# Kernel optimization log

Measured on AMD Instinct MI355X. Metric: run time of the kernel, lower is better.

The kernel has to match this reference:

```python
import jax, jax.numpy as jnp
import numpy as np

# dims
B, C, H, W = 8, 256, 64, 128
P = 4                      # patch size (p1 == p2)
E = C // 2                 # embed dim = ngf//2 = Mamba d_model
HP, WP = H // P, W // P
N = HP * WP                # 512 tokens
DM = E                     # Mamba d_model
DI = 2 * DM                # d_inner (expand=2)
DS = 16                    # d_state
DC = 4                     # d_conv
DR = DM // 16              # dt_rank
NG = 128                   # new_ngf
S = 2                      # pixel-shuffle stride


def setup_inputs() -> dict:
    key = jax.random.key(0)
    ks = jax.random.split(key, 16)
    g = lambda i, shape, s=0.02: jax.random.normal(ks[i], shape, jnp.float32) * s
    return {
        'x': jax.random.normal(ks[0], (B, C, H, W), jnp.float32),
        # patch embed (conv k=stride=P)
        'patch_w': g(1, (E, C, P, P)),
        'patch_b': jnp.zeros((E,), jnp.float32),
        # Mamba params
        'in_proj_w': g(2, (2 * DI, DM)),
        'conv1d_w': g(3, (DI, DC), 0.1),
        'conv1d_b': jnp.zeros((DI,), jnp.float32),
        'x_proj_w': g(4, (DR + 2 * DS, DI)),
        'dt_proj_w': g(5, (DI, DR), 0.1),
        'dt_proj_b': jnp.full((DI,), -3.0, jnp.float32),
        'A_log': jnp.log(jnp.broadcast_to(jnp.arange(1, DS + 1, dtype=jnp.float32), (DI, DS))),
        'D_param': jnp.ones((DI,), jnp.float32),
        'out_proj_w': g(6, (DM, DI)),
        # unpatchify linear N -> N*P*P
        'lin_w': g(7, (N * P * P, N)),
        'lin_b': jnp.zeros((N * P * P,), jnp.float32),
        # nerv conv (3x3, out = new_ngf*S*S)
        'conv_w': g(8, (NG * S * S, E, 3, 3), 0.05),
        'conv_b': jnp.zeros((NG * S * S,), jnp.float32),
        # residual FFN (1x1)
        'ffn_w1': g(9, (NG, NG)),
        'ffn_b1': jnp.zeros((NG,), jnp.float32),
        'ffn_w2': g(10, (NG, NG)),
        'ffn_b2': jnp.zeros((NG,), jnp.float32),
    }


def reference(x, patch_w, patch_b, in_proj_w, conv1d_w, conv1d_b, x_proj_w,
              dt_proj_w, dt_proj_b, A_log, D_param, out_proj_w, lin_w, lin_b,
              conv_w, conv_b, ffn_w1, ffn_b1, ffn_w2, ffn_b2):
    silu = jax.nn.silu
    # ---- patch embed: (B,C,H,W) -> (B,N,E)
    t = jax.lax.conv_general_dilated(x, patch_w, (P, P), 'VALID',
                                     dimension_numbers=('NCHW', 'OIHW', 'NCHW'))
    t = t + patch_b[None, :, None, None]
    t = t.reshape(B, E, N).transpose(0, 2, 1)  # (B,N,E)

    # ---- Mamba selective scan
    xz = jnp.einsum('bld,ed->ble', t, in_proj_w)      # (B,N,2*DI)
    xin, z = jnp.split(xz, 2, axis=-1)
    # depthwise causal conv1d over sequence
    xp = jnp.pad(xin, ((0, 0), (DC - 1, 0), (0, 0)))
    xc = sum(xp[:, k:k + N, :] * conv1d_w[:, k] for k in range(DC)) + conv1d_b
    xc = silu(xc)                                     # (B,N,DI)
    dbl = jnp.einsum('bld,ed->ble', xc, x_proj_w)
    dt, Bs, Cs = dbl[..., :DR], dbl[..., DR:DR + DS], dbl[..., DR + DS:]
    dt = jax.nn.softplus(jnp.einsum('blr,dr->bld', dt, dt_proj_w) + dt_proj_b)
    A = -jnp.exp(A_log)                               # (DI,DS)
    dA = jnp.exp(dt[..., None] * A)                   # (B,N,DI,DS)
    dBx = dt[..., None] * Bs[:, :, None, :] * xc[..., None]

    def step(h, inputs):
        dA_t, dBx_t, C_t = inputs
        h = dA_t * h + dBx_t                          # (B,DI,DS)
        y = jnp.einsum('bdn,bn->bd', h, C_t)
        return h, y

    h0 = jnp.zeros((B, DI, DS), xc.dtype)
    _, ys = jax.lax.scan(step, h0, (dA.transpose(1, 0, 2, 3),
                                    dBx.transpose(1, 0, 2, 3),
                                    Cs.transpose(1, 0, 2)))
    y = ys.transpose(1, 0, 2) + D_param * xc
    y = y * silu(z)
    out = jnp.einsum('bld,ed->ble', y, out_proj_w)    # (B,N,DM)

    # ---- unpatchify: (B,N,E) -> (B,E,H,W)
    u = out.transpose(0, 2, 1)                        # (B,E,N)
    u = jnp.einsum('ben,mn->bem', u, lin_w) + lin_b   # (B,E,N*P*P)
    u = u.reshape(B, E, HP, WP, P, P).transpose(0, 1, 2, 4, 3, 5)
    u = u.reshape(B, E, H, W)

    # ---- nerv block: 3x3 conv -> pixel shuffle -> gelu
    c = jax.lax.conv_general_dilated(u, conv_w, (1, 1), ((1, 1), (1, 1)),
                                     dimension_numbers=('NCHW', 'OIHW', 'NCHW'))
    c = c + conv_b[None, :, None, None]               # (B,NG*S*S,H,W)
    c = c.reshape(B, NG, S, S, H, W).transpose(0, 1, 4, 2, 5, 3)
    c = c.reshape(B, NG, H * S, W * S)
    c = jax.nn.gelu(c)

    # ---- residual FFN (1x1 convs over channels)
    f = jax.nn.gelu(jnp.einsum('bchw,ec->behw', c, ffn_w1) + ffn_b1[None, :, None, None])
    f = jnp.einsum('behw,ce->bchw', f, ffn_w2) + ffn_b2[None, :, None, None]
    return c + f
```

## Files before the change

### kernel.cpp

```cpp
#include <hip/hip_runtime.h>
#include <hip/hip_bf16.h>

#define HW2 32768

typedef __attribute__((ext_vector_type(8))) short short8v;
typedef __attribute__((ext_vector_type(4))) float f32x4;

__device__ __forceinline__ float siluf(float x){ return x / (1.f + __expf(-x)); }
__device__ __forceinline__ float geluf(float v){
  float t = 0.7978845608028654f * fmaf(0.044715f*v*v, v, v);
  t = fminf(fmaxf(t, -15.f), 15.f);
  float e = __expf(2.f*t);
  return 0.5f*v*(1.f + (e-1.f)/(e+1.f));
}
__device__ __forceinline__ ushort bf16rne(float f){
  unsigned u = __float_as_uint(f);
  unsigned r = (u + 0x7fffu + ((u >> 16) & 1u)) >> 16;
  return (ushort)r;
}
__device__ __forceinline__ float bf2f(ushort u){ return __uint_as_float(((unsigned)u) << 16); }
__device__ __forceinline__ void split2(float v, ushort& h, ushort& lo){
  h = bf16rne(v);
  lo = bf16rne(v - bf2f(h));
}

__global__ __launch_bounds__(256) void k_zero4(uint4* __restrict__ p, int n){
  int i = blockIdx.x*256 + threadIdx.x;
  if (i < n) p[i] = make_uint4(0,0,0,0);
}

__global__ __launch_bounds__(256) void k_wprep(const float* __restrict__ cw, ushort* __restrict__ wbf){
  int idx = blockIdx.x*256 + threadIdx.x;
  int j    = idx & 7;
  int lane = (idx >> 3) & 63;
  int f    = (idx >> 9) & 3;
  int tap  = (idx >> 11) % 9;
  int rest = idx / 18432;
  int ec = rest & 3, ocg = rest >> 2;
  int o = ocg*64 + f*16 + (lane & 15);
  int e = ec*32 + (lane >> 4)*8 + j;
  float v = cw[((size_t)o*128 + e)*9 + tap];
  wbf[idx] = bf16rne(v);
}

__global__ __launch_bounds__(256) void k_wffn(const float* __restrict__ w1, const float* __restrict__ w2,
                                              ushort* __restrict__ wpad){
  int idx = blockIdx.x*256 + threadIdx.x;
  int which = idx / 17408;
  int rem = idx - which*17408;
  int e = rem / 136, k = rem - e*136;
  const float* s = which ? w2 : w1;
  wpad[idx] = (k < 128) ? bf16rne(s[e*128 + k]) : (ushort)0;
}

__global__ __launch_bounds__(256) void k_wlin(const float* __restrict__ lw, ushort* __restrict__ lwbf){
  int i = blockIdx.x*256 + threadIdx.x;
  float4 v = reinterpret_cast<const float4*>(lw)[i];
  uint2 u;
  u.x = (uint)bf16rne(v.x) | ((uint)bf16rne(v.y) << 16);
  u.y = (uint)bf16rne(v.z) | ((uint)bf16rne(v.w) << 16);
  reinterpret_cast<uint2*>(lwbf)[i] = u;
}

__global__ __launch_bounds__(256) void k_ytr(const float* __restrict__ yo, ushort* __restrict__ ybfT){
  __shared__ float tile[32][132];
  int b = blockIdx.x, n0 = blockIdx.y*32;
  int tid = threadIdx.x;
  for (int it = 0; it < 16; ++it) {
    int idx = it*256 + tid;
    int row = idx >> 7, e = idx & 127;
    tile[row][e] = yo[((size_t)(b*512 + n0 + row))*128 + e];
  }
  __syncthreads();
  int e = tid >> 1, half = tid & 1;
  uint* dst = reinterpret_cast<uint*>(ybfT + ((size_t)b*128 + e)*512 + n0 + half*16);
  #pragma unroll
  for (int j = 0; j < 8; ++j) {
    int n = half*16 + j*2;
    dst[j] = (uint)bf16rne(tile[n][e]) | ((uint)bf16rne(tile[n+1][e]) << 16);
  }
}

__global__ __launch_bounds__(256) void k_patchm(const float* __restrict__ x, const float* __restrict__ pw,
                                                float* __restrict__ part){
  __shared__ ushort Ah[4096], Al[4096], Wh[4096], Wl[4096];
  int m0 = blockIdx.x * 128;
  int ks = blockIdx.y;
  int tid = threadIdx.x;
  int l = tid & 63, wv = tid >> 6;
  int wm = wv >> 1, we = wv & 1;
  int lj = l & 15, lg = l >> 4;
  f32x4 acc[4][4];
  #pragma unroll
  for (int a = 0; a < 4; ++a)
    #pragma unroll
    for (int b = 0; b < 4; ++b)
      acc[a][b] = (f32x4){0.f,0.f,0.f,0.f};
  int kbase = ks * 512;

  for (int it = 0; it < 16; ++it) {
    int k0 = kbase + it*32;
    __syncthreads();
    #pragma unroll
    for (int q = 0; q < 4; ++q) {
      int flat = q*256 + tid;
      int row = flat & 127, kk4 = flat >> 7;
      int m = m0 + row;
      int bb = m >> 9, ll = m & 511;
      int hp = ll >> 5, wp = ll & 31;
      int k = k0 + kk4*4;
      int c = k >> 4, i2 = (k >> 2) & 3;
      float4 v = *reinterpret_cast<const float4*>(x + (((bb*256 + c)*64 + hp*4 + i2)*128 + wp*4));
      ushort h0,h1,h2,h3,q0,q1,q2,q3;
      split2(v.x,h0,q0); split2(v.y,h1,q1); split2(v.z,h2,q2); split2(v.w,h3,q3);
      uint2 uh, ul;
      uh.x = (uint)h0 | ((uint)h1 << 16); uh.y = (uint)h2 | ((uint)h3 << 16);
      ul.x = (uint)q0 | ((uint)q1 << 16); ul.y = (uint)q2 | ((uint)q3 << 16);
      int lane = ((kk4 >> 1) << 4) | (row & 15);
      int dst = ((row >> 4)*64 + lane)*8 + (kk4 & 1)*4;
      *reinterpret_cast<uint2*>(Ah + dst) = uh;
      *reinterpret_cast<uint2*>(Al + dst) = ul;
    }
    #pragma unroll
    for (int q = 0; q < 4; ++q) {
      int flat = q*256 + tid;
      int e = flat >> 3, kk4 = flat & 7;
      float4 v = *reinterpret_cast<const float4*>(pw + (size_t)e*4096 + k0 + kk4*4);
      ushort h0,h1,h2,h3,q0,q1,q2,q3;
      split2(v.x,h0,q0); split2(v.y,h1,q1); split2(v.z,h2,q2); split2(v.w,h3,q3);
      uint2 uh, ul;
      uh.x = (uint)h0 | ((uint)h1 << 16); uh.y = (uint)h2 | ((uint)h3 << 16);
      ul.x = (uint)q0 | ((uint)q1 << 16); ul.y = (uint)q2 | ((uint)q3 << 16);
      int lane = ((kk4 >> 1) << 4) | (e & 15);
      int dst = ((e >> 4)*64 + lane)*8 + (kk4 & 1)*4;
      *reinterpret_cast<uint2*>(Wh + dst) = uh;
      *reinterpret_cast<uint2*>(Wl + dst) = ul;
    }
    __syncthreads();

    short8v ah[4], al_[4], wh[4], wl_[4];
    #pragma unroll
    for (int f = 0; f < 4; ++f) {
      ah[f]  = *reinterpret_cast<const short8v*>(Ah + ((wm*4 + f)*64 + l)*8);
      al_[f] = *reinterpret_cast<const short8v*>(Al + ((wm*4 + f)*64 + l)*8);
      wh[f]  = *reinterpret_cast<const short8v*>(Wh + ((we*4 + f)*64 + l)*8);
      wl_[f] = *reinterpret_cast<const short8v*>(Wl + ((we*4 + f)*64 + l)*8);
    }
    #pragma unroll
    for (int fo = 0; fo < 4; ++fo)
      #pragma unroll
      for (int fj = 0; fj < 4; ++fj) {
        acc[fo][fj] = __builtin_amdgcn_mfma_f32_16x16x32_bf16(ah[fo],  wh[fj],  acc[fo][fj], 0, 0, 0);
        acc[fo][fj] = __builtin_amdgcn_mfma_f32_16x16x32_bf16(ah[fo],  wl_[fj], acc[fo][fj], 0, 0, 0);
        acc[fo][fj] = __builtin_amdgcn_mfma_f32_16x16x32_bf16(al_[fo], wh[fj],  acc[fo][fj], 0, 0, 0);
      }
  }
  float* pb = part + (size_t)ks*524288;
  #pragma unroll
  for (int fo = 0; fo < 4; ++fo) {
    int m = m0 + wm*64 + fo*16 + lg*4;
    #pragma unroll
    for (int fj = 0; fj < 4; ++fj) {
      int e = we*64 + fj*16 + lj;
      f32x4 a = acc[fo][fj];
      pb[(size_t)(m+0)*128 + e] = a.x;
      pb[(size_t)(m+1)*128 + e] = a.y;
      pb[(size_t)(m+2)*128 + e] = a.z;
      pb[(size_t)(m+3)*128 + e] = a.w;
    }
  }
}

__global__ __launch_bounds__(256) void k_tred(const float* __restrict__ part, const float* __restrict__ pb,
                                              float* __restrict__ t){
  int i = blockIdx.x*256 + threadIdx.x;
  const float4* p4 = reinterpret_cast<const float4*>(part);
  float4 s = reinterpret_cast<const float4*>(pb)[i & 31];
  #pragma unroll
  for (int ks = 0; ks < 8; ++ks) {
    float4 v = p4[(size_t)ks*131072 + i];
    s.x += v.x; s.y += v.y; s.z += v.z; s.w += v.w;
  }
  reinterpret_cast<float4*>(t)[i] = s;
}

__global__ __launch_bounds__(256) void k_gemm(const float* __restrict__ A, const float* __restrict__ W,
                                              float* __restrict__ C, int M, int N, int K){
  __shared__ __align__(16) float As[16][68];
  __shared__ __align__(16) float Bs[16][68];
  int m0 = blockIdx.x * 64, n0 = blockIdx.y * 64;
  int tid = threadIdx.x;
  int tm = tid >> 4, tn = tid & 15;
  int lm = tid >> 2, kq = tid & 3;
  float acc[4][4] = {};
  const float* Abase = A + (size_t)(m0 + lm)*K + kq*4;
  const float* Wbase = W + (size_t)(n0 + lm)*K + kq*4;
  for (int k0 = 0; k0 < K; k0 += 16) {
    float4 av = *reinterpret_cast<const float4*>(Abase + k0);
    float4 bv = *reinterpret_cast<const float4*>(Wbase + k0);
    As[kq*4+0][lm]=av.x; As[kq*4+1][lm]=av.y; As[kq*4+2][lm]=av.z; As[kq*4+3][lm]=av.w;
    Bs[kq*4+0][lm]=bv.x; Bs[kq*4+1][lm]=bv.y; Bs[kq*4+2][lm]=bv.z; Bs[kq*4+3][lm]=bv.w;
    __syncthreads();
    #pragma unroll
    for (int kk = 0; kk < 16; ++kk) {
      float4 a = *reinterpret_cast<const float4*>(&As[kk][tm*4]);
      float4 b = *reinterpret_cast<const float4*>(&Bs[kk][tn*4]);
      float ar[4] = {a.x,a.y,a.z,a.w};
      float br[4] = {b.x,b.y,b.z,b.w};
      #pragma unroll
      for (int i = 0; i < 4; ++i)
        #pragma unroll
        for (int j = 0; j < 4; ++j)
          acc[i][j] = fmaf(ar[i], br[j], acc[i][j]);
    }
    __syncthreads();
  }
  #pragma unroll
  for (int i = 0; i < 4; ++i) {
    float4 ov = make_float4(acc[i][0], acc[i][1], acc[i][2], acc[i][3]);
    *reinterpret_cast<float4*>(C + (size_t)(m0 + tm*4 + i)*N + n0 + tn*4) = ov;
  }
}

__global__ __launch_bounds__(256) void k_conv1d(const float* __restrict__ xz, const float* __restrict__ w,
                                                const float* __restrict__ bias, float* __restrict__ xc){
  int idx = blockIdx.x*256 + threadIdx.x;
  int d = idx & 255;
  int l = (idx >> 8) & 511;
  int bb = idx >> 17;
  const float* base = xz + (size_t)bb*512*512 + d;
  float s = bias[d];
  #pragma unroll
  for (int k = 0; k < 4; ++k) {
    int ls = l - 3 + k;
    if (ls >= 0) s = fmaf(base[(size_t)ls*512], w[d*4+k], s);
  }
  xc[idx] = s / (1.f + __expf(-s));
}

__global__ __launch_bounds__(256) void k_xproj(const float* __restrict__ xc, const float* __restrict__ xpw,
                                               const float* __restrict__ dtw, const float* __restrict__ dtb,
                                               float* __restrict__ dbl, float* __restrict__ dt){
  __shared__ __align__(16) float sxc[256];
  __shared__ float sdbl[40];
  int bl = blockIdx.x;
  int tid = threadIdx.x;
  sxc[tid] = xc[(size_t)bl*256 + tid];
  __syncthreads();
  if (tid < 40) {
    const float4* wr = reinterpret_cast<const float4*>(xpw + tid*256);
    const float4* xr = reinterpret_cast<const float4*>(sxc);
    float s = 0.f;
    #pragma unroll 8
    for (int i = 0; i < 64; ++i) {
      float4 w = wr[i], xv = xr[i];
      s += w.x*xv.x + w.y*xv.y + w.z*xv.z + w.w*xv.w;
    }
    sdbl[tid] = s;
    dbl[(size_t)bl*40 + tid] = s;
  }
  __syncthreads();
  float s = dtb[tid];
  const float* wr = dtw + tid*8;
  #pragma unroll
  for (int r = 0; r < 8; ++r) s = fmaf(sdbl[r], wr[r], s);
  float sp = (s > 20.f) ? s : log1pf(__expf(s));
  dt[(size_t)bl*256 + tid] = sp;
}

__global__ __launch_bounds__(256) void k_scanA(const float* __restrict__ dt, const float* __restrict__ dbl,
                                               const float* __restrict__ xc, const float* __restrict__ A_log,
                                               float* __restrict__ aprod, float* __restrict__ hend){
  __shared__ float sdt[32][16], sxc[32][16], sB[32][16];
  int tid = threadIdx.x;
  int bg = blockIdx.x;
  int ch = blockIdx.y;
  int bb = bg >> 4, dgrp = bg & 15;
  int l0 = ch*32;
  #pragma unroll
  for (int it = 0; it < 2; ++it) {
    int idx = it*256 + tid;
    int t = idx >> 4, dd = idx & 15;
    int base = bb*512 + l0 + t;
    sdt[t][dd] = dt[(size_t)base*256 + dgrp*16 + dd];
    sxc[t][dd] = xc[(size_t)base*256 + dgrp*16 + dd];
    sB [t][dd] = dbl[(size_t)base*40 + 8 + dd];
  }
  __syncthreads();
  int n = tid & 15, dloc = tid >> 4;
  float Ac = -__expf(A_log[(dgrp*16 + dloc)*16 + n]);
  float a = 1.f, h = 0.f;
  #pragma unroll
  for (int t = 0; t < 32; ++t) {
    float dtv = sdt[t][dloc], xcv = sxc[t][dloc], Bv = sB[t][n];
    float dA = __expf(dtv*Ac);
    h = fmaf(dA, h, dtv*Bv*xcv);
    a *= dA;
  }
  aprod[(size_t)(bg*16 + ch)*256 + tid] = a;
  hend [(size_t)(bg*16 + ch)*256 + tid] = h;
}

__global__ __launch_bounds__(256) void k_scanB(const float* __restrict__ aprod, const float* __restrict__ hend,
                                               float* __restrict__ hstart){
  int tid = threadIdx.x;
  int bg = blockIdx.x;
  float hs = 0.f;
  #pragma unroll
  for (int ch = 0; ch < 16; ++ch) {
    size_t idx = (size_t)(bg*16 + ch)*256 + tid;
    hstart[idx] = hs;
    hs = fmaf(aprod[idx], hs, hend[idx]);
  }
}

__global__ __launch_bounds__(256) void k_scanC(const float* __restrict__ dt, const float* __restrict__ dbl,
                                               const float* __restrict__ xc, const float* __restrict__ xz,
                                               const float* __restrict__ A_log, const float* __restrict__ Dp,
                                               const float* __restrict__ hstart, float* __restrict__ y){
  __shared__ float sdt[32][16], sxc[32][16], sB[32][16], sC[32][16], sz[32][16];
  int tid = threadIdx.x;
  int bg = blockIdx.x;
  int ch = blockIdx.y;
  int bb = bg >> 4, dgrp = bg & 15;
  int l0 = ch*32;
  #pragma unroll
  for (int it = 0; it < 2; ++it) {
    int idx = it*256 + tid;
    int t = idx >> 4, dd = idx & 15;
    int base = bb*512 + l0 + t;
    sdt[t][dd] = dt[(size_t)base*256 + dgrp*16 + dd];
    sxc[t][dd] = xc[(size_t)base*256 + dgrp*16 + dd];
    sB [t][dd] = dbl[(size_t)base*40 + 8  + dd];
    sC [t][dd] = dbl[(size_t)base*40 + 24 + dd];
    sz [t][dd] = xz[(size_t)base*512 + 256 + dgrp*16 + dd];
  }
  __syncthreads();
  int n = tid & 15, dloc = tid >> 4;
  int d = dgrp*16 + dloc;
  float Ac = -__expf(A_log[d*16 + n]);
  float Dv = Dp[d];
  float h = hstart[(size_t)(bg*16 + ch)*256 + tid];
  #pragma unroll 4
  for (int t = 0; t < 32; ++t) {
    float dtv = sdt[t][dloc], xcv = sxc[t][dloc];
    float Bv = sB[t][n], Cv = sC[t][n];
    float dA = __expf(dtv*Ac);
    h = fmaf(dA, h, dtv*Bv*xcv);
    float yp = h*Cv;
    yp += __shfl_xor(yp, 1, 16);
    yp += __shfl_xor(yp, 2, 16);
    yp += __shfl_xor(yp, 4, 16);
    yp += __shfl_xor(yp, 8, 16);
    if (n == 0) {
      float zv = sz[t][dloc];
      y[(size_t)(bb*512 + l0 + t)*256 + d] = (yp + Dv*xcv) * (zv / (1.f + __expf(-zv)));
    }
  }
}

__global__ __launch_bounds__(512) void k_linm(const ushort* __restrict__ ybfT, const ushort* __restrict__ lwbf,
                                              const float* __restrict__ lb, ushort* __restrict__ ubf){
  __shared__ ushort As[128*88];
  __shared__ ushort Bs[128*88];
  int m0 = blockIdx.x * 128;
  int b  = blockIdx.y;
  int tid = threadIdx.x;
  int l = tid & 63, wv = tid >> 6;
  int wm = wv & 3, we = wv >> 2;
  int lj = l & 15, lg = l >> 4;
  f32x4 acc[4][2];
  #pragma unroll
  for (int fo = 0; fo < 4; ++fo)
    #pragma unroll
    for (int fj = 0; fj < 2; ++fj)
      acc[fo][fj] = (f32x4){0.f,0.f,0.f,0.f};

  for (int k0 = 0; k0 < 512; k0 += 64) {
    __syncthreads();
    #pragma unroll
    for (int it = 0; it < 2; ++it) {
      int flat = it*512 + tid;
      int e = flat >> 3, kc8 = flat & 7;
      *reinterpret_cast<uint4*>(&As[e*88 + kc8*8]) =
        *reinterpret_cast<const uint4*>(ybfT + ((size_t)b*128 + e)*512 + k0 + kc8*8);
      *reinterpret_cast<uint4*>(&Bs[e*88 + kc8*8]) =
        *reinterpret_cast<const uint4*>(lwbf + (size_t)(m0 + e)*512 + k0 + kc8*8);
    }
    __syncthreads();
    #pragma unroll
    for (int kc = 0; kc < 2; ++kc) {
      short8v af[4], bq[2];
      #pragma unroll
      for (int fo = 0; fo < 4; ++fo)
        af[fo] = *reinterpret_cast<const short8v*>(&As[(we*64 + fo*16 + lj)*88 + kc*32 + lg*8]);
      #pragma unroll
      for (int fj = 0; fj < 2; ++fj)
        bq[fj] = *reinterpret_cast<const short8v*>(&Bs[(wm*32 + fj*16 + lj)*88 + kc*32 + lg*8]);
      #pragma unroll
      for (int fo = 0; fo < 4; ++fo)
        #pragma unroll
        for (int fj = 0; fj < 2; ++fj)
          acc[fo][fj] = __builtin_amdgcn_mfma_f32_16x16x32_bf16(af[fo], bq[fj], acc[fo][fj], 0, 0, 0);
    }
  }
  #pragma unroll
  for (int fj = 0; fj < 2; ++fj) {
    int m = m0 + wm*32 + fj*16 + lj;
    float bias = lb[m];
    int hh = ((m >> 9) << 2) + ((m >> 2) & 3);
    int ww = (((m >> 4) & 31) << 2) + (m & 3);
    #pragma unroll
    for (int fo = 0; fo < 4; ++fo) {
      int eg = we*2 + (fo >> 1);
      int e5 = ((fo & 1) << 4) + (lg << 2);
      f32x4 a = acc[fo][fj];
      uint2 u;
      u.x = (uint)bf16rne(a.x + bias) | ((uint)bf16rne(a.y + bias) << 16);
      u.y = (uint)bf16rne(a.z + bias) | ((uint)bf16rne(a.w + bias) << 16);
      *reinterpret_cast<uint2*>(ubf + ((((size_t)b*4 + eg)*66 + hh + 1)*130 + ww + 1)*32 + e5) = u;
    }
  }
}

__global__ __launch_bounds__(256, 3) void k_conv3m(const ushort* __restrict__ ubf, const ushort* __restrict__ wbf,
                                                   const float* __restrict__ cb, float* __restrict__ out){
  __shared__ ushort wlds[18432];
  int h2 = blockIdx.x;
  int bz = blockIdx.y;
  int bb = bz >> 3, ocg = bz & 7;
  int tid = threadIdx.x;
  int l   = tid & 63;
  int wv  = tid >> 6;
  int hr  = wv >> 1;
  int wseg = (wv & 1) * 64;
  int lj = l & 15, lg = l >> 4;

  f32x4 acc[4][4];
  #pragma unroll
  for (int i = 0; i < 4; ++i)
    #pragma unroll
    for (int j = 0; j < 4; ++j)
      acc[i][j] = (f32x4){0.f, 0.f, 0.f, 0.f};

  for (int ec = 0; ec < 4; ++ec) {
    __syncthreads();
    const uint4* sA = reinterpret_cast<const uint4*>(wbf) + (size_t)(ocg*4 + ec)*2304;
    uint4* dA = reinterpret_cast<uint4*>(wlds);
    #pragma unroll
    for (int q = 0; q < 9; ++q) dA[q*256 + tid] = sA[q*256 + tid];
    __syncthreads();

    const ushort* ub_ec = ubf + (((size_t)(bb*4 + ec)*66 + 2*h2 + hr)*130 + wseg + lj)*32 + lg*8;
    #pragma unroll
    for (int ki = 0; ki < 3; ++ki) {
      const ushort* bbase = ub_ec + (size_t)ki*4160;
      #pragma unroll
      for (int kj = 0; kj < 3; ++kj) {
        const ushort* wtap = wlds + (ki*3 + kj)*2048 + l*8;
        short8v af[4], bfr[4];
        #pragma unroll
        for (int f = 0; f < 4; ++f)
          af[f] = *reinterpret_cast<const short8v*>(wtap + f*512);
        #pragma unroll
        for (int f = 0; f < 4; ++f)
          bfr[f] = *reinterpret_cast<const short8v*>(bbase + (f*16 + kj)*32);
        #pragma unroll
        for (int fo = 0; fo < 4; ++fo)
          #pragma unroll
          for (int fj = 0; fj < 4; ++fj)
            acc[fo][fj] = __builtin_amdgcn_mfma_f32_16x16x32_bf16(af[fo], bfr[fj], acc[fo][fj], 0, 0, 0);
      }
    }
  }

  int row = h2*2 + hr;
  #pragma unroll
  for (int fo = 0; fo < 4; ++fo) {
    int obase = ocg*64 + fo*16 + lg*4;
    int g = obase >> 2;
    float b0 = cb[obase], b1 = cb[obase+1], b2 = cb[obase+2], b3 = cb[obase+3];
    size_t rbase0 = (((size_t)bb*128 + g)*128 + 2*row)*256;
    size_t rbase1 = rbase0 + 256;
    #pragma unroll
    for (int fj = 0; fj < 4; ++fj) {
      int w = wseg + fj*16 + lj;
      f32x4 a = acc[fo][fj];
      float2 v0 = make_float2(geluf(a.x + b0), geluf(a.y + b1));
      float2 v1 = make_float2(geluf(a.z + b2), geluf(a.w + b3));
      *reinterpret_cast<float2*>(out + rbase0 + 2*w) = v0;
      *reinterpret_cast<float2*>(out + rbase1 + 2*w) = v1;
    }
  }
}

__global__ __launch_bounds__(512) void k_ffnm(const ushort* __restrict__ wpad, const float* __restrict__ b1,
                                              const float* __restrict__ b2, float* __restrict__ io){
  extern __shared__ ushort sm[];
  ushort* cT = sm;
  ushort* wl = sm + 128*136;
  int pix0 = blockIdx.x * 128;
  int bb = pix0 >> 15;
  int hw0 = pix0 & 32767;
  int tid = threadIdx.x;
  int l = tid & 63, wv = tid >> 6;
  int wc = wv >> 2, wp = wv & 3;
  int lj = l & 15, lg = l >> 4;
  int r = tid & 1, hpair = tid >> 1;
  const float* cbase = io + (size_t)bb*128*HW2 + hw0;

  for (int it = 0; it < 16; ++it) {
    int flat = it*256 + hpair;
    int pp = flat & 63;
    int cpair = flat >> 6;
    int ch = cpair*2 + r;
    float2 v = *reinterpret_cast<const float2*>(cbase + (size_t)ch*HW2 + pp*2);
    float oa = __shfl_xor(v.x, 1);
    float ob = __shfl_xor(v.y, 1);
    ushort lo = r ? bf16rne(ob) : bf16rne(v.x);
    ushort hi = r ? bf16rne(v.y) : bf16rne(oa);
    *reinterpret_cast<uint*>(&cT[(pp*2 + r)*136 + cpair*2]) = (uint)lo | ((uint)hi << 16);
  }
  {
    const uint4* src = reinterpret_cast<const uint4*>(wpad);
    uint4* dst = reinterpret_cast<uint4*>(wl);
    for (int i = tid; i < 2176; i += 512) dst[i] = src[i];
  }
  __syncthreads();

  f32x4 acc[4][2];
  #pragma unroll
  for (int fo = 0; fo < 4; ++fo)
    #pragma unroll
    for (int fj = 0; fj < 2; ++fj)
      acc[fo][fj] = (f32x4){0.f,0.f,0.f,0.f};

  #pragma unroll
  for (int kc = 0; kc < 4; ++kc) {
    short8v af[4], bq[2];
    #pragma unroll
    for (int fo = 0; fo < 4; ++fo)
      af[fo] = *reinterpret_cast<const short8v*>(&wl[(wc*64 + fo*16 + lj)*136 + kc*32 + lg*8]);
    #pragma unroll
    for (int fj = 0; fj < 2; ++fj)
      bq[fj] = *reinterpret_cast<const short8v*>(&cT[(wp*32 + fj*16 + lj)*136 + kc*32 + lg*8]);
    #pragma unroll
    for (int fo = 0; fo < 4; ++fo)
      #pragma unroll
      for (int fj = 0; fj < 2; ++fj)
        acc[fo][fj] = __builtin_amdgcn_mfma_f32_16x16x32_bf16(af[fo], bq[fj], acc[fo][fj], 0, 0, 0);
  }
  __syncthreads();

  const ushort* w2g = wpad + 17408;
  short8v a2[4], a2n[4];
  #pragma unroll
  for (int fo = 0; fo < 4; ++fo)
    a2[fo] = *reinterpret_cast<const short8v*>(w2g + (size_t)(wc*64 + fo*16 + lj)*136 + lg*8);

  #pragma unroll
  for (int fo = 0; fo < 4; ++fo) {
    int ch0 = wc*64 + fo*16 + lg*4;
    float c0 = b1[ch0], c1 = b1[ch0+1], c2 = b1[ch0+2], c3 = b1[ch0+3];
    #pragma unroll
    for (int fj = 0; fj < 2; ++fj) {
      int px = wp*32 + fj*16 + lj;
      f32x4 a = acc[fo][fj];
      uint2 u;
      u.x = (uint)bf16rne(geluf(a.x + c0)) | ((uint)bf16rne(geluf(a.y + c1)) << 16);
      u.y = (uint)bf16rne(geluf(a.z + c2)) | ((uint)bf16rne(geluf(a.w + c3)) << 16);
      *reinterpret_cast<uint2*>(&wl[px*136 + ch0]) = u;
    }
  }
  __syncthreads();

  #pragma unroll
  for (int fo = 0; fo < 4; ++fo)
    #pragma unroll
    for (int fj = 0; fj < 2; ++fj)
      acc[fo][fj] = (f32x4){0.f,0.f,0.f,0.f};

  #pragma unroll
  for (int kc = 0; kc < 4; ++kc) {
    if (kc < 3) {
      #pragma unroll
      for (int fo = 0; fo < 4; ++fo)
        a2n[fo] = *reinterpret_cast<const short8v*>(w2g + (size_t)(wc*64 + fo*16 + lj)*136 + (kc+1)*32 + lg*8);
    }
    short8v bq[2];
    #pragma unroll
    for (int fj = 0; fj < 2; ++fj)
      bq[fj] = *reinterpret_cast<const short8v*>(&wl[(wp*32 + fj*16 + lj)*136 + kc*32 + lg*8]);
    #pragma unroll
    for (int fo = 0; fo < 4; ++fo)
      #pragma unroll
      for (int fj = 0; fj < 2; ++fj)
        acc[fo][fj] = __builtin_amdgcn_mfma_f32_16x16x32_bf16(a2[fo], bq[fj], acc[fo][fj], 0, 0, 0);
    #pragma unroll
    for (int fo = 0; fo < 4; ++fo) a2[fo] = a2n[fo];
  }

  #pragma unroll
  for (int fo = 0; fo < 4; ++fo) {
    int ch0 = wc*64 + fo*16 + lg*4;
    float d0 = b2[ch0], d1 = b2[ch0+1], d2 = b2[ch0+2], d3 = b2[ch0+3];
    #pragma unroll
    for (int fj = 0; fj < 2; ++fj) {
      int px = wp*32 + fj*16 + lj;
      f32x4 a = acc[fo][fj];
      uint2 cu = *reinterpret_cast<const uint2*>(&cT[px*136 + ch0]);
      float cv0 = __uint_as_float((cu.x & 0xffffu) << 16);
      float cv1 = __uint_as_float(cu.x & 0xffff0000u);
      float cv2 = __uint_as_float((cu.y & 0xffffu) << 16);
      float cv3 = __uint_as_float(cu.y & 0xffff0000u);
      float* p0 = io + (size_t)bb*128*HW2 + (size_t)ch0*HW2 + hw0 + px;
      p0[0]             = cv0 + a.x + d0;
      p0[HW2]           = cv1 + a.y + d1;
      p0[2*HW2]         = cv2 + a.z + d2;
      p0[3*(size_t)HW2] = cv3 + a.w + d3;
    }
  }
}

extern "C" void kernel_launch(void* const* d_in, const int* in_sizes, int n_in,
                              void* d_out, int out_size, void* d_ws, size_t ws_size,
                              hipStream_t stream) {
  const float* x          = (const float*)d_in[0];
  const float* patch_w    = (const float*)d_in[1];
  const float* patch_b    = (const float*)d_in[2];
  const float* in_proj_w  = (const float*)d_in[3];
  const float* conv1d_w   = (const float*)d_in[4];
  const float* conv1d_b   = (const float*)d_in[5];
  const float* x_proj_w   = (const float*)d_in[6];
  const float* dt_proj_w  = (const float*)d_in[7];
  const float* dt_proj_b  = (const float*)d_in[8];
  const float* A_log      = (const float*)d_in[9];
  const float* D_param    = (const float*)d_in[10];
  const float* out_proj_w = (const float*)d_in[11];
  const float* lin_w      = (const float*)d_in[12];
  const float* lin_b      = (const float*)d_in[13];
  const float* conv_w     = (const float*)d_in[14];
  const float* conv_b     = (const float*)d_in[15];
  const float* ffn_w1     = (const float*)d_in[16];
  const float* ffn_b1     = (const float*)d_in[17];
  const float* ffn_w2     = (const float*)d_in[18];
  const float* ffn_b2     = (const float*)d_in[19];
  float* out = (float*)d_out;
  float* ws  = (float*)d_ws;

  float* t    = ws;
  float* xz   = t    + 524288;
  float* xc   = xz   + 2097152;
  float* dbl  = xc   + 1048576;
  float* dt   = dbl  + 163840;
  float* y    = dt   + 1048576;
  float* yo   = y    + 1048576;
  float* apr  = yo   + 524288;
  float* hend = apr  + 524288;
  float* hst  = hend + 524288;
  ushort* ubf  = (ushort*)(hst + 524288);
  ushort* wbf  = ubf + 10982400;
  ushort* wpad = wbf + 589824;
  ushort* lwbf = wpad + 34816;
  ushort* ybfT = lwbf + 4194304;
  float* part = xz;

  k_zero4 <<<dim3(5363), dim3(256), 0, stream>>>((uint4*)ubf, 1372800);
  k_wprep <<<dim3(2304), dim3(256), 0, stream>>>(conv_w, wbf);
  k_wffn  <<<dim3(136), dim3(256), 0, stream>>>(ffn_w1, ffn_w2, wpad);
  k_wlin  <<<dim3(4096), dim3(256), 0, stream>>>(lin_w, lwbf);
  k_patchm<<<dim3(32, 8), dim3(256), 0, stream>>>(x, patch_w, part);
  k_tred  <<<dim3(512), dim3(256), 0, stream>>>(part, patch_b, t);
  k_gemm  <<<dim3(64, 8), dim3(256), 0, stream>>>(t, in_proj_w, xz, 4096, 512, 128);
  k_conv1d<<<dim3(4096), dim3(256), 0, stream>>>(xz, conv1d_w, conv1d_b, xc);
  k_xproj <<<dim3(4096), dim3(256), 0, stream>>>(xc, x_proj_w, dt_proj_w, dt_proj_b, dbl, dt);
  k_scanA <<<dim3(128, 16), dim3(256), 0, stream>>>(dt, dbl, xc, A_log, apr, hend);
  k_scanB <<<dim3(128), dim3(256), 0, stream>>>(apr, hend, hst);
  k_scanC <<<dim3(128, 16), dim3(256), 0, stream>>>(dt, dbl, xc, xz, A_log, D_param, hst, y);
  k_gemm  <<<dim3(64, 2), dim3(256), 0, stream>>>(y, out_proj_w, yo, 4096, 128, 256);
  k_ytr   <<<dim3(8, 16), dim3(256), 0, stream>>>(yo, ybfT);
  k_linm  <<<dim3(64, 8), dim3(512), 0, stream>>>(ybfT, lwbf, lin_b, ubf);
  k_conv3m<<<dim3(32, 64), dim3(256), 0, stream>>>(ubf, wbf, conv_b, out);
  k_ffnm  <<<dim3(2048), dim3(512), (size_t)(2*128*136)*sizeof(ushort), stream>>>(wpad, ffn_b1, ffn_b2, out);
}
```

Measured before the change: 344.9 us.

## Write conv output as bf16 intermediate, split conv+FFN into batch halves

The 3x3 conv now writes its gelu output as bf16 into a workspace buffer instead of fp32 into the final output, and the FFN reads that bf16 buffer and writes the final fp32 result. This halves conv write traffic and FFN read traffic and may keep the intermediate resident in cache. Conv and FFN run in two batch halves of four so the intermediate is smaller. The full zeroing of the padded buffer is replaced by a kernel that zeroes only the halo border, and conv launch bounds rise to four blocks per SM. The result is unchanged in value, because the FFN already rounded its input to bf16.

```diff
diff --git a/kernel.cpp b/kernel.cpp
--- a/kernel.cpp
+++ b/kernel.cpp
@@ -24,9 +24,23 @@
   lo = bf16rne(v - bf2f(h));
 }
 
-__global__ __launch_bounds__(256) void k_zero4(uint4* __restrict__ p, int n){
-  int i = blockIdx.x*256 + threadIdx.x;
-  if (i < n) p[i] = make_uint4(0,0,0,0);
+__global__ __launch_bounds__(256) void k_zb(uint4* __restrict__ ubf4){
+  int bid = blockIdx.x;
+  int tid = threadIdx.x;
+  uint4 z = make_uint4(0,0,0,0);
+  size_t base4 = (size_t)bid * 34320;
+  for (int i = tid; i < 1552; i += 256) {
+    size_t off;
+    if (i < 520)       off = i;
+    else if (i < 1040) off = 33800 + (i - 520);
+    else {
+      int j = i - 1040;
+      int row = 1 + (j >> 3);
+      int colsel = (j >> 2) & 1, q = j & 3;
+      off = (size_t)row*520 + colsel*516 + q;
+    }
+    ubf4[base4 + off] = z;
+  }
 }
 
 __global__ __launch_bounds__(256) void k_wprep(const float* __restrict__ cw, ushort* __restrict__ wbf){
@@ -423,12 +437,14 @@
   }
 }
 
-__global__ __launch_bounds__(256, 3) void k_conv3m(const ushort* __restrict__ ubf, const ushort* __restrict__ wbf,
-                                                   const float* __restrict__ cb, float* __restrict__ out){
+__global__ __launch_bounds__(256, 4) void k_conv3m(const ushort* __restrict__ ubf, const ushort* __restrict__ wbf,
+                                                   const float* __restrict__ cb, ushort* __restrict__ cbf,
+                                                   int bbase){
   __shared__ ushort wlds[18432];
   int h2 = blockIdx.x;
   int bz = blockIdx.y;
-  int bb = bz >> 3, ocg = bz & 7;
+  int bbl = bz >> 3, ocg = bz & 7;
+  int bb = bbase + bbl;
   int tid = threadIdx.x;
   int l   = tid & 63;
   int wv  = tid >> 6;
@@ -454,7 +470,7 @@
     const ushort* ub_ec = ubf + (((size_t)(bb*4 + ec)*66 + 2*h2 + hr)*130 + wseg + lj)*32 + lg*8;
     #pragma unroll
     for (int ki = 0; ki < 3; ++ki) {
-      const ushort* bbase = ub_ec + (size_t)ki*4160;
+      const ushort* bbase_p = ub_ec + (size_t)ki*4160;
       #pragma unroll
       for (int kj = 0; kj < 3; ++kj) {
         const ushort* wtap = wlds + (ki*3 + kj)*2048 + l*8;
@@ -464,7 +480,7 @@
           af[f] = *reinterpret_cast<const short8v*>(wtap + f*512);
         #pragma unroll
         for (int f = 0; f < 4; ++f)
-          bfr[f] = *reinterpret_cast<const short8v*>(bbase + (f*16 + kj)*32);
+          bfr[f] = *reinterpret_cast<const short8v*>(bbase_p + (f*16 + kj)*32);
         #pragma unroll
         for (int fo = 0; fo < 4; ++fo)
           #pragma unroll
@@ -480,46 +496,47 @@
     int obase = ocg*64 + fo*16 + lg*4;
     int g = obase >> 2;
     float b0 = cb[obase], b1 = cb[obase+1], b2 = cb[obase+2], b3 = cb[obase+3];
-    size_t rbase0 = (((size_t)bb*128 + g)*128 + 2*row)*256;
+    size_t rbase0 = (((size_t)bbl*128 + g)*128 + 2*row)*256;
     size_t rbase1 = rbase0 + 256;
     #pragma unroll
     for (int fj = 0; fj < 4; ++fj) {
       int w = wseg + fj*16 + lj;
       f32x4 a = acc[fo][fj];
-      float2 v0 = make_float2(geluf(a.x + b0), geluf(a.y + b1));
-      float2 v1 = make_float2(geluf(a.z + b2), geluf(a.w + b3));
-      *reinterpret_cast<float2*>(out + rbase0 + 2*w) = v0;
-      *reinterpret_cast<float2*>(out + rbase1 + 2*w) = v1;
+      uint u0 = (uint)bf16rne(geluf(a.x + b0)) | ((uint)bf16rne(geluf(a.y + b1)) << 16);
+      uint u1 = (uint)bf16rne(geluf(a.z + b2)) | ((uint)bf16rne(geluf(a.w + b3)) << 16);
+      *reinterpret_cast<uint*>(cbf + rbase0 + 2*w) = u0;
+      *reinterpret_cast<uint*>(cbf + rbase1 + 2*w) = u1;
     }
   }
 }
 
 __global__ __launch_bounds__(512) void k_ffnm(const ushort* __restrict__ wpad, const float* __restrict__ b1,
-                                              const float* __restrict__ b2, float* __restrict__ io){
+                                              const float* __restrict__ b2, const ushort* __restrict__ cbf,
+                                              float* __restrict__ out, int bbase){
   extern __shared__ ushort sm[];
   ushort* cT = sm;
   ushort* wl = sm + 128*136;
   int pix0 = blockIdx.x * 128;
-  int bb = pix0 >> 15;
+  int bbl = pix0 >> 15;
+  int bb = bbase + bbl;
   int hw0 = pix0 & 32767;
   int tid = threadIdx.x;
   int l = tid & 63, wv = tid >> 6;
   int wc = wv >> 2, wp = wv & 3;
   int lj = l & 15, lg = l >> 4;
   int r = tid & 1, hpair = tid >> 1;
-  const float* cbase = io + (size_t)bb*128*HW2 + hw0;
+  const ushort* cbase = cbf + (size_t)bbl*128*HW2 + hw0;
 
   for (int it = 0; it < 16; ++it) {
     int flat = it*256 + hpair;
     int pp = flat & 63;
     int cpair = flat >> 6;
     int ch = cpair*2 + r;
-    float2 v = *reinterpret_cast<const float2*>(cbase + (size_t)ch*HW2 + pp*2);
-    float oa = __shfl_xor(v.x, 1);
-    float ob = __shfl_xor(v.y, 1);
-    ushort lo = r ? bf16rne(ob) : bf16rne(v.x);
-    ushort hi = r ? bf16rne(v.y) : bf16rne(oa);
-    *reinterpret_cast<uint*>(&cT[(pp*2 + r)*136 + cpair*2]) = (uint)lo | ((uint)hi << 16);
+    uint own = *reinterpret_cast<const uint*>(cbase + (size_t)ch*HW2 + pp*2);
+    uint other = __shfl_xor((int)own, 1);
+    uint o = r ? ((other >> 16) | (own & 0xffff0000u))
+               : ((own & 0xffffu) | (other << 16));
+    *reinterpret_cast<uint*>(&cT[(pp*2 + r)*136 + cpair*2]) = o;
   }
   {
     const uint4* src = reinterpret_cast<const uint4*>(wpad);
@@ -613,7 +630,7 @@
       float cv1 = __uint_as_float(cu.x & 0xffff0000u);
       float cv2 = __uint_as_float((cu.y & 0xffffu) << 16);
       float cv3 = __uint_as_float(cu.y & 0xffff0000u);
-      float* p0 = io + (size_t)bb*128*HW2 + (size_t)ch0*HW2 + hw0 + px;
+      float* p0 = out + (size_t)bb*128*HW2 + (size_t)ch0*HW2 + hw0 + px;
       p0[0]             = cv0 + a.x + d0;
       p0[HW2]           = cv1 + a.y + d1;
       p0[2*HW2]         = cv2 + a.z + d2;
@@ -646,9 +663,11 @@
   const float* ffn_w2     = (const float*)d_in[18];
   const float* ffn_b2     = (const float*)d_in[19];
   float* out = (float*)d_out;
-  float* ws  = (float*)d_ws;
-
-  float* t    = ws;
+
+  ushort* ubf  = (ushort*)d_ws;
+  ushort* wbf  = ubf + 10982400;
+  ushort* wpad = wbf + 589824;
+  float* t    = (float*)(wpad + 34816);
   float* xz   = t    + 524288;
   float* xc   = xz   + 2097152;
   float* dbl  = xc   + 1048576;
@@ -658,14 +677,12 @@
   float* apr  = yo   + 524288;
   float* hend = apr  + 524288;
   float* hst  = hend + 524288;
-  ushort* ubf  = (ushort*)(hst + 524288);
-  ushort* wbf  = ubf + 10982400;
-  ushort* wpad = wbf + 589824;
-  ushort* lwbf = wpad + 34816;
+  ushort* lwbf = (ushort*)(hst + 524288);
   ushort* ybfT = lwbf + 4194304;
   float* part = xz;
-
-  k_zero4 <<<dim3(5363), dim3(256), 0, stream>>>((uint4*)ubf, 1372800);
+  ushort* cbf = (ushort*)t;
+
+  k_zb    <<<dim3(32), dim3(256), 0, stream>>>((uint4*)ubf);
   k_wprep <<<dim3(2304), dim3(256), 0, stream>>>(conv_w, wbf);
   k_wffn  <<<dim3(136), dim3(256), 0, stream>>>(ffn_w1, ffn_w2, wpad);
   k_wlin  <<<dim3(4096), dim3(256), 0, stream>>>(lin_w, lwbf);
@@ -680,6 +697,8 @@
   k_gemm  <<<dim3(64, 2), dim3(256), 0, stream>>>(y, out_proj_w, yo, 4096, 128, 256);
   k_ytr   <<<dim3(8, 16), dim3(256), 0, stream>>>(yo, ybfT);
   k_linm  <<<dim3(64, 8), dim3(512), 0, stream>>>(ybfT, lwbf, lin_b, ubf);
-  k_conv3m<<<dim3(32, 64), dim3(256), 0, stream>>>(ubf, wbf, conv_b, out);
-  k_ffnm  <<<dim3(2048), dim3(512), (size_t)(2*128*136)*sizeof(ushort), stream>>>(wpad, ffn_b1, ffn_b2, out);
-}
+  k_conv3m<<<dim3(32, 32), dim3(256), 0, stream>>>(ubf, wbf, conv_b, cbf, 0);
+  k_ffnm  <<<dim3(1024), dim3(512), (size_t)(2*128*136)*sizeof(ushort), stream>>>(wpad, ffn_b1, ffn_b2, cbf, out, 0);
+  k_conv3m<<<dim3(32, 32), dim3(256), 0, stream>>>(ubf, wbf, conv_b, cbf, 4);
+  k_ffnm  <<<dim3(1024), dim3(512), (size_t)(2*128*136)*sizeof(ushort), stream>>>(wpad, ffn_b1, ffn_b2, cbf, out, 4);
+}
```

Result: slower. 364.8 us (+5.8%).
